# Kernel tuning notes

Measured on AMD Instinct MI355X. Metric: run time of the kernel, lower is better.

## Reference

```python
import math
import jax, jax.numpy as jnp
import numpy as np

B, CIN, COUT, K, S = 2, 64, 64, 3, 18  # batch, channels, kernel size per dim, spatial size per dim


def setup_inputs() -> dict:
    key = jax.random.key(0)
    k1, k2 = jax.random.split(key)
    inputs = jax.random.normal(k1, (B, CIN, S, S, S, S), dtype=jnp.float32)
    std = 1.0 / math.sqrt(CIN * K ** 4)  # matches init_weight: 1/sqrt(in_channels * n_offsets)
    kernel = jax.random.uniform(k2, (K ** 4, CIN, COUT), dtype=jnp.float32, minval=-std, maxval=std)
    return {"inputs": inputs, "kernel": kernel}


def reference(inputs, kernel):
    # kernel: [k0*k1*k2*k3, Cin, Cout], offsets enumerated row-major over the 4 kernel dims.
    # Equivalent to the per-offset matmul + shift-accumulate in conv4d (valid padding,
    # stride=1, dilation=1), expressed as a single 4-spatial-dim XLA convolution.
    cin, cout = kernel.shape[1], kernel.shape[2]
    w = kernel.reshape(K, K, K, K, cin, cout).transpose(5, 4, 0, 1, 2, 3)  # OIWXYZ
    out = jax.lax.conv_general_dilated(
        inputs, w,
        window_strides=(1, 1, 1, 1),
        padding='VALID',
        rhs_dilation=(1, 1, 1, 1),
        dimension_numbers=('NCWXYZ', 'OIWXYZ', 'NCWXYZ'),
    )  # [B, Cout, 16, 16, 16, 16]
    return out
```

## Files before the change

### kernel.cpp

```cpp
#include <hip/hip_runtime.h>


typedef __attribute__((ext_vector_type(8))) short bf16x8;
typedef __attribute__((ext_vector_type(4))) float f32x4;
typedef __attribute__((ext_vector_type(8))) unsigned short ushort8;
typedef unsigned short u16;
typedef unsigned int u32;

#define S_OFF_BYTES 663552u
#define WS_NEEDED   27537408u

__device__ __forceinline__ u16 f2bf(float f) {
    u32 u = __float_as_uint(f);
    u += 0x7FFFu + ((u >> 16) & 1u);
    return (u16)(u >> 16);
}

__global__ __launch_bounds__(256) void wprep(const float* __restrict__ ker, u16* __restrict__ wg) {
    const int g = blockIdx.x * 256 + threadIdx.x;
    const int l = g & 63, ks = (g >> 6) & 1, rt = (g >> 7) & 3, off = g >> 9;
    const int co  = rt * 16 + (l & 15);
    const int ci0 = ks * 32 + (l >> 4) * 8;
    const float* p = ker + (size_t)off * 4096 + co;
    ushort8 v;
#pragma unroll
    for (int e = 0; e < 8; ++e) v[e] = f2bf(p[(size_t)(ci0 + e) * 64]);
    *(ushort8*)(wg + (size_t)g * 8) = v;
}

__global__ __launch_bounds__(256) void sprep(const float* __restrict__ in, u16* __restrict__ s) {
    __shared__ u16 L[64 * 330];
    const int blk = blockIdx.x;
    const int b = blk / 324, wx = blk - b * 324;
    const float* src = in + (size_t)b * 6718464 + (wx / 18) * 5832 + (wx % 18) * 324;
    const int t = threadIdx.x;
    for (int i = t; i < 5184; i += 256) {
        const int ci = i / 81, j = i - ci * 81;
        float4 v = *(const float4*)(src + (size_t)ci * 104976 + j * 4);
        u32* q = (u32*)&L[ci * 330 + j * 4];
        q[0] = f2bf(v.x) | ((u32)f2bf(v.y) << 16);
        q[1] = f2bf(v.z) | ((u32)f2bf(v.w) << 16);
    }
    __syncthreads();
    u16* dst = s + (size_t)blk * 20736;
    for (int i = t; i < 2592; i += 256) {
        const int ks = i / 1296, r4 = i - ks * 1296;
        const int rem = r4 >> 2, g = r4 & 3;
        ushort8 v;
#pragma unroll
        for (int e = 0; e < 8; ++e) v[e] = L[(ks * 32 + g * 8 + e) * 330 + rem];
        const int gp = g ^ ((rem >> 1) & 3);
        *(ushort8*)(dst + ks * 10368 + rem * 32 + gp * 8) = v;
    }
}

__global__ __launch_bounds__(256, 2)
void conv4d_main(const u16* __restrict__ wg, const u16* __restrict__ s, float* __restrict__ out) {
    __shared__ u16 T[2][324 * 32];

    const int bid = blockIdx.x;
    const int bs  = (bid & 7) * 64 + (bid >> 3);
    const int b   = bs >> 8;
    const int w   = (bs >> 4) & 15;
    const int x   = bs & 15;

    const int t  = threadIdx.x, wv = t >> 6, l = t & 63;
    const int lg = l >> 4, ll = l & 15;

    f32x4 acc[4][4];
#pragma unroll
    for (int i = 0; i < 4; ++i)
#pragma unroll
        for (int j = 0; j < 4; ++j) acc[i][j] = (f32x4){0.f, 0.f, 0.f, 0.f};

    const u16* sb = s + (size_t)(b * 324 + w * 18 + x) * 20736;

#define STAGE(p, bufi)                                                               \
    do {                                                                             \
        const int kwx_ = (p) >> 1, ks_ = (p) & 1;                                    \
        const int kw_ = kwx_ / 3, kx_ = kwx_ - kw_ * 3;                              \
        const u16* src_ = sb + (size_t)(kw_ * 18 + kx_) * 20736 + ks_ * 10368;       \
        for (int i_ = t; i_ < 1296; i_ += 256)                                       \
            __builtin_amdgcn_global_load_lds(                                        \
                (const __attribute__((address_space(1))) u32*)(src_ + i_ * 8),       \
                (__attribute__((address_space(3))) u32*)&T[bufi][i_ * 8], 16, 0, 0); \
    } while (0)

    STAGE(0, 0);
    __syncthreads();

    int buf = 0;
    for (int p = 0; p < 18; ++p) {
        if (p + 1 < 18) STAGE(p + 1, buf ^ 1);

        const int kwx = p >> 1, ks = p & 1;
        const u16* wo = wg + (size_t)(kwx * 9) * 4096 + ks * 512;
        const u16* Tb = T[buf];

        bf16x8 a[4][4];
#pragma unroll
        for (int i = 0; i < 3; ++i)
#pragma unroll
            for (int rt = 0; rt < 4; ++rt)
                a[i][rt] = *(const bf16x8*)(wo + (size_t)i * 4096 + (size_t)rt * 1024 + l * 8);

#pragma unroll
        for (int sub = 0; sub < 9; ++sub) {
            if (sub + 3 < 9) {
                const u16* wn = wo + (size_t)(sub + 3) * 4096;
#pragma unroll
                for (int rt = 0; rt < 4; ++rt)
                    a[(sub + 3) & 3][rt] = *(const bf16x8*)(wn + (size_t)rt * 1024 + l * 8);
            }
            const int ky = sub / 3, kz = sub - ky * 3;
            bf16x8 bfr[4];
#pragma unroll
            for (int ct = 0; ct < 4; ++ct) {
                const int rem = (4 * wv + ct + ky) * 18 + ll + kz;
                bfr[ct] = *(const bf16x8*)&Tb[rem * 32 + ((lg ^ ((rem >> 1) & 3)) << 3)];
            }
            __builtin_amdgcn_s_setprio(1);
#pragma unroll
            for (int ct = 0; ct < 4; ++ct)
#pragma unroll
                for (int rt = 0; rt < 4; ++rt)
                    acc[rt][ct] = __builtin_amdgcn_mfma_f32_16x16x32_bf16(
                        a[sub & 3][rt], bfr[ct], acc[rt][ct], 0, 0, 0);
            __builtin_amdgcn_s_setprio(0);
        }
        __syncthreads();
        buf ^= 1;
    }
#undef STAGE

    float* ob = out + (size_t)b * 4194304 + (size_t)w * 4096 + (size_t)x * 256;
#pragma unroll
    for (int rt = 0; rt < 4; ++rt) {
        const int co0 = rt * 16 + 4 * lg;
#pragma unroll
        for (int ct = 0; ct < 4; ++ct) {
            const int base = (4 * wv + ct) * 16 + ll;
#pragma unroll
            for (int r = 0; r < 4; ++r)
                ob[(size_t)(co0 + r) * 65536 + base] = acc[rt][ct][r];
        }
    }
}

__global__ __launch_bounds__(512, 2)
void conv4d_mfma(const float* __restrict__ in, const float* __restrict__ ker,
                 float* __restrict__ out) {
    __shared__ unsigned short T[18 * 18 * 64];
    __shared__ unsigned short Wt[2][64 * 64];
    const int bx = blockIdx.x;
    const int b = bx >> 8, wsp = (bx >> 4) & 15, x = bx & 15;
    const int t = threadIdx.x, wv = t >> 6, l = t & 63;
    const int lg = l >> 4, ll = l & 15;
    const float* inb = in + (size_t)b * 6718464 + wsp * 5832 + x * 324;
    f32x4 acc[4][2];
#pragma unroll
    for (int i = 0; i < 4; ++i)
#pragma unroll
        for (int j = 0; j < 2; ++j) acc[i][j] = (f32x4){0.f, 0.f, 0.f, 0.f};
#pragma unroll
    for (int f0 = 0; f0 < 4096; f0 += 512) {
        const int f = f0 + t, ci = f >> 6, co = f & 63;
        Wt[0][co * 64 + ((((ci >> 3) ^ (co & 7)) << 3) | (ci & 7))] = f2bf(ker[f]);
    }
    for (int off = 0; off < 81; ++off) {
        const int sub = off % 9;
        if (sub == 0) {
            const int kw = off / 27, kx = (off / 9) % 3;
            const float* p = inb + kw * 5832 + kx * 324;
            for (int f = t; f < 18 * 18 * 64; f += 512) {
                const int ci = f / 324, rem = f - ci * 324, zp = rem % 18;
                T[rem * 64 + ((((ci >> 3) ^ (zp & 7)) << 3) | (ci & 7))] =
                    f2bf(p[(size_t)ci * 104976 + rem]);
            }
        }
        if (off + 1 < 81) {
            const float* p = ker + (off + 1) * 4096;
            unsigned short* wb = Wt[(off + 1) & 1];
#pragma unroll
            for (int f0 = 0; f0 < 4096; f0 += 512) {
                const int f = f0 + t, ci = f >> 6, co = f & 63;
                wb[co * 64 + ((((ci >> 3) ^ (co & 7)) << 3) | (ci & 7))] = f2bf(p[f]);
            }
        }
        if (sub == 0) __syncthreads();
        const int ky = sub / 3, kz = sub - ky * 3;
        const int zp = ll + kz, zs = zp & 7;
#pragma unroll
        for (int ks = 0; ks < 2; ++ks) {
            bf16x8 af[4];
#pragma unroll
            for (int rt = 0; rt < 4; ++rt)
                af[rt] = *(const bf16x8*)&Wt[off & 1][(rt * 16 + ll) * 64 + (((lg + 4 * ks) ^ (ll & 7)) << 3)];
#pragma unroll
            for (int ct = 0; ct < 2; ++ct) {
                const int rem = (2 * wv + ct + ky) * 18 + zp;
                const bf16x8 bfr = *(const bf16x8*)&T[rem * 64 + (((lg + 4 * ks) ^ zs) << 3)];
#pragma unroll
                for (int rt = 0; rt < 4; ++rt)
                    acc[rt][ct] = __builtin_amdgcn_mfma_f32_16x16x32_bf16(af[rt], bfr, acc[rt][ct], 0, 0, 0);
            }
        }
        __syncthreads();
    }
    float* ob = out + (size_t)b * 4194304 + wsp * 4096 + x * 256;
#pragma unroll
    for (int rt = 0; rt < 4; ++rt) {
        const int co0 = rt * 16 + 4 * lg;
#pragma unroll
        for (int ct = 0; ct < 2; ++ct) {
            const int base = (2 * wv + ct) * 16 + ll;
#pragma unroll
            for (int r = 0; r < 4; ++r)
                ob[(size_t)(co0 + r) * 65536 + base] = acc[rt][ct][r];
        }
    }
}

extern "C" void kernel_launch(void* const* d_in, const int* in_sizes, int n_in,
                              void* d_out, int out_size, void* d_ws, size_t ws_size,
                              hipStream_t stream) {
    const float* in  = (const float*)d_in[0];
    const float* ker = (const float*)d_in[1];
    float* out = (float*)d_out;
    if (ws_size >= (size_t)WS_NEEDED) {
        u16* wg = (u16*)d_ws;
        u16* s  = (u16*)((char*)d_ws + S_OFF_BYTES);
        wprep<<<dim3(162), dim3(256), 0, stream>>>(ker, wg);
        sprep<<<dim3(648), dim3(256), 0, stream>>>(in, s);
        conv4d_main<<<dim3(512), dim3(256), 0, stream>>>(wg, s, out);
    } else {
        conv4d_mfma<<<dim3(512), dim3(512), 0, stream>>>(in, ker, out);
    }
}
```

Baseline: 99.26 us.

## Split channel halves across two wave groups with staggered 4-slot staging and LDS reduction

Doubles the conv4d_main block to 512 threads, with waves 0-3 handling the first input-channel half and waves 4-7 the second. The two groups are staggered by one stage over a 4-slot LDS ring, and each barrier step stages two slices. At the end the second group writes its partial accumulators to LDS and the first group adds them before storing. This aims to double the waves available to hide load and MFMA latency per block, at the cost of more LDS per block, an extra reduction pass, and idle waves in the first and last steps.

```diff
diff --git a/kernel.cpp b/kernel.cpp
--- a/kernel.cpp
+++ b/kernel.cpp
@@ -54,9 +54,9 @@
     }
 }
 
-__global__ __launch_bounds__(256, 2)
+__global__ __launch_bounds__(512, 4)
 void conv4d_main(const u16* __restrict__ wg, const u16* __restrict__ s, float* __restrict__ out) {
-    __shared__ u16 T[2][324 * 32];
+    __shared__ u16 R[4][324 * 32];
 
     const int bid = blockIdx.x;
     const int bs  = (bid & 7) * 64 + (bid >> 3);
@@ -64,8 +64,10 @@
     const int w   = (bs >> 4) & 15;
     const int x   = bs & 15;
 
-    const int t  = threadIdx.x, wv = t >> 6, l = t & 63;
-    const int lg = l >> 4, ll = l & 15;
+    const int tid = threadIdx.x, wv = tid >> 6, l = tid & 63;
+    const int ks  = wv >> 2;
+    const int g   = wv & 3;
+    const int lg  = l >> 4, ll = l & 15;
 
     f32x4 acc[4][4];
 #pragma unroll
@@ -75,74 +77,91 @@
 
     const u16* sb = s + (size_t)(b * 324 + w * 18 + x) * 20736;
 
-#define STAGE(p, bufi)                                                               \
+#define STAGE_H(h)                                                                   \
     do {                                                                             \
-        const int kwx_ = (p) >> 1, ks_ = (p) & 1;                                    \
-        const int kw_ = kwx_ / 3, kx_ = kwx_ - kw_ * 3;                              \
-        const u16* src_ = sb + (size_t)(kw_ * 18 + kx_) * 20736 + ks_ * 10368;       \
-        for (int i_ = t; i_ < 1296; i_ += 256)                                       \
-            __builtin_amdgcn_global_load_lds(                                        \
-                (const __attribute__((address_space(1))) u32*)(src_ + i_ * 8),       \
-                (__attribute__((address_space(3))) u32*)&T[bufi][i_ * 8], 16, 0, 0); \
+        if ((h) <= 17) {                                                             \
+            const int kwx_ = (h) >> 1, ksh_ = (h) & 1;                               \
+            const int kw_ = kwx_ / 3, kx_ = kwx_ - kw_ * 3;                          \
+            const u16* src_ = sb + (size_t)(kw_ * 18 + kx_) * 20736 + ksh_ * 10368;  \
+            u16* dst_ = &R[(h) & 3][0];                                              \
+            for (int i_ = tid; i_ < 1296; i_ += 512)                                 \
+                __builtin_amdgcn_global_load_lds(                                    \
+                    (const __attribute__((address_space(1))) u32*)(src_ + i_ * 8),   \
+                    (__attribute__((address_space(3))) u32*)(dst_ + i_ * 8),         \
+                    16, 0, 0);                                                       \
+        }                                                                            \
     } while (0)
 
-    STAGE(0, 0);
+    STAGE_H(0);
     __syncthreads();
 
-    int buf = 0;
-    for (int p = 0; p < 18; ++p) {
-        if (p + 1 < 18) STAGE(p + 1, buf ^ 1);
-
-        const int kwx = p >> 1, ks = p & 1;
-        const u16* wo = wg + (size_t)(kwx * 9) * 4096 + ks * 512;
-        const u16* Tb = T[buf];
-
-        bf16x8 a[4][4];
-#pragma unroll
-        for (int i = 0; i < 3; ++i)
+    for (int t = 0; t < 10; ++t) {
+        STAGE_H(2 * t + 1);
+        STAGE_H(2 * t + 2);
+
+        const int h = 2 * t - ks;
+        if (h >= 0 && h <= 17) {
+            const int kwx = h >> 1;
+            const u16* Tb = R[h & 3];
+            const u16* wo = wg + (size_t)(kwx * 9) * 4096 + ks * 512;
+
+            bf16x8 a[2][4];
 #pragma unroll
             for (int rt = 0; rt < 4; ++rt)
-                a[i][rt] = *(const bf16x8*)(wo + (size_t)i * 4096 + (size_t)rt * 1024 + l * 8);
-
-#pragma unroll
-        for (int sub = 0; sub < 9; ++sub) {
-            if (sub + 3 < 9) {
-                const u16* wn = wo + (size_t)(sub + 3) * 4096;
-#pragma unroll
-                for (int rt = 0; rt < 4; ++rt)
-                    a[(sub + 3) & 3][rt] = *(const bf16x8*)(wn + (size_t)rt * 1024 + l * 8);
-            }
-            const int ky = sub / 3, kz = sub - ky * 3;
-            bf16x8 bfr[4];
+                a[0][rt] = *(const bf16x8*)(wo + (size_t)rt * 1024 + l * 8);
+
+#pragma unroll
+            for (int sub = 0; sub < 9; ++sub) {
+                if (sub + 1 < 9) {
+                    const u16* wn = wo + (size_t)(sub + 1) * 4096;
+#pragma unroll
+                    for (int rt = 0; rt < 4; ++rt)
+                        a[(sub + 1) & 1][rt] = *(const bf16x8*)(wn + (size_t)rt * 1024 + l * 8);
+                }
+                const int ky = sub / 3, kz = sub - ky * 3;
+                bf16x8 bfr[4];
+#pragma unroll
+                for (int ct = 0; ct < 4; ++ct) {
+                    const int rem = (4 * g + ct + ky) * 18 + ll + kz;
+                    bfr[ct] = *(const bf16x8*)&Tb[rem * 32 + ((lg ^ ((rem >> 1) & 3)) << 3)];
+                }
+                __builtin_amdgcn_s_setprio(1);
+#pragma unroll
+                for (int ct = 0; ct < 4; ++ct)
+#pragma unroll
+                    for (int rt = 0; rt < 4; ++rt)
+                        acc[rt][ct] = __builtin_amdgcn_mfma_f32_16x16x32_bf16(
+                            a[sub & 1][rt], bfr[ct], acc[rt][ct], 0, 0, 0);
+                __builtin_amdgcn_s_setprio(0);
+            }
+        }
+        __syncthreads();
+    }
+#undef STAGE_H
+
+    float* rbuf = (float*)&R[0][0];
+    if (ks == 1) {
+#pragma unroll
+        for (int rt = 0; rt < 4; ++rt)
+#pragma unroll
+            for (int ct = 0; ct < 4; ++ct)
+                *(f32x4*)&rbuf[g * 4096 + (rt * 4 + ct) * 256 + l * 4] = acc[rt][ct];
+    }
+    __syncthreads();
+    if (ks == 0) {
+        float* ob = out + (size_t)b * 4194304 + (size_t)w * 4096 + (size_t)x * 256;
+#pragma unroll
+        for (int rt = 0; rt < 4; ++rt) {
+            const int co0 = rt * 16 + 4 * lg;
 #pragma unroll
             for (int ct = 0; ct < 4; ++ct) {
-                const int rem = (4 * wv + ct + ky) * 18 + ll + kz;
-                bfr[ct] = *(const bf16x8*)&Tb[rem * 32 + ((lg ^ ((rem >> 1) & 3)) << 3)];
-            }
-            __builtin_amdgcn_s_setprio(1);
-#pragma unroll
-            for (int ct = 0; ct < 4; ++ct)
-#pragma unroll
-                for (int rt = 0; rt < 4; ++rt)
-                    acc[rt][ct] = __builtin_amdgcn_mfma_f32_16x16x32_bf16(
-                        a[sub & 3][rt], bfr[ct], acc[rt][ct], 0, 0, 0);
-            __builtin_amdgcn_s_setprio(0);
-        }
-        __syncthreads();
-        buf ^= 1;
-    }
-#undef STAGE
-
-    float* ob = out + (size_t)b * 4194304 + (size_t)w * 4096 + (size_t)x * 256;
-#pragma unroll
-    for (int rt = 0; rt < 4; ++rt) {
-        const int co0 = rt * 16 + 4 * lg;
-#pragma unroll
-        for (int ct = 0; ct < 4; ++ct) {
-            const int base = (4 * wv + ct) * 16 + ll;
-#pragma unroll
-            for (int r = 0; r < 4; ++r)
-                ob[(size_t)(co0 + r) * 65536 + base] = acc[rt][ct][r];
+                f32x4 v = *(const f32x4*)&rbuf[g * 4096 + (rt * 4 + ct) * 256 + l * 4];
+                v = v + acc[rt][ct];
+                const int base = (4 * g + ct) * 16 + ll;
+#pragma unroll
+                for (int r = 0; r < 4; ++r)
+                    ob[(size_t)(co0 + r) * 65536 + base] = v[r];
+            }
         }
     }
 }
@@ -232,7 +251,7 @@
         u16* s  = (u16*)((char*)d_ws + S_OFF_BYTES);
         wprep<<<dim3(162), dim3(256), 0, stream>>>(ker, wg);
         sprep<<<dim3(648), dim3(256), 0, stream>>>(in, s);
-        conv4d_main<<<dim3(512), dim3(256), 0, stream>>>(wg, s, out);
+        conv4d_main<<<dim3(512), dim3(512), 0, stream>>>(wg, s, out);
     } else {
         conv4d_mfma<<<dim3(512), dim3(512), 0, stream>>>(in, ker, out);
     }
```

Measured after the change: 99.04 us. Within noise of the previous version (-0.2%).

## Triple-buffer LDS input staging with explicit vmcnt waits instead of syncthreads

Applied to the files above, without the earlier changes.

Replaces the double-buffered shared-memory tile with a three-slot ring. Each phase now prefetches the slab two phases ahead instead of one. The full `__syncthreads` is replaced by a partial `s_waitcnt vmcnt` plus a raw `s_barrier`, so the block waits only for the slab about to be consumed. Each wave now issues a fixed, unrolled set of direct-to-LDS loads over its own quarter of the tile. This deepens latency hiding for the global-to-LDS copies, at the cost of about 20 KB more LDS per block and a hand-tuned vmcnt count that depends on the exact number of in-flight loads.

```diff
diff --git a/kernel.cpp b/kernel.cpp
--- a/kernel.cpp
+++ b/kernel.cpp
@@ -56,7 +56,7 @@
 
 __global__ __launch_bounds__(256, 2)
 void conv4d_main(const u16* __restrict__ wg, const u16* __restrict__ s, float* __restrict__ out) {
-    __shared__ u16 T[2][324 * 32];
+    __shared__ u16 R[3][324 * 32];
 
     const int bid = blockIdx.x;
     const int bs  = (bid & 7) * 64 + (bid >> 3);
@@ -75,27 +75,39 @@
 
     const u16* sb = s + (size_t)(b * 324 + w * 18 + x) * 20736;
 
-#define STAGE(p, bufi)                                                               \
-    do {                                                                             \
-        const int kwx_ = (p) >> 1, ks_ = (p) & 1;                                    \
-        const int kw_ = kwx_ / 3, kx_ = kwx_ - kw_ * 3;                              \
-        const u16* src_ = sb + (size_t)(kw_ * 18 + kx_) * 20736 + ks_ * 10368;       \
-        for (int i_ = t; i_ < 1296; i_ += 256)                                       \
-            __builtin_amdgcn_global_load_lds(                                        \
-                (const __attribute__((address_space(1))) u32*)(src_ + i_ * 8),       \
-                (__attribute__((address_space(3))) u32*)&T[bufi][i_ * 8], 16, 0, 0); \
+#define STAGE_U(h, slot)                                                                 \
+    do {                                                                                 \
+        const int kwx_ = (h) >> 1, ks_ = (h) & 1;                                        \
+        const int kw_ = kwx_ / 3, kx_ = kwx_ - kw_ * 3;                                  \
+        const u16* src_ = sb + (size_t)(kw_ * 18 + kx_) * 20736 + ks_ * 10368;           \
+        const int base_ = wv * 324;                                                      \
+        _Pragma("unroll")                                                                \
+        for (int k_ = 0; k_ < 5; ++k_) {                                                 \
+            const int i_ = base_ + k_ * 64 + l;                                          \
+            __builtin_amdgcn_global_load_lds(                                            \
+                (const __attribute__((address_space(1))) u32*)(src_ + (size_t)i_ * 8),   \
+                (__attribute__((address_space(3))) u32*)&R[slot][i_ * 8], 16, 0, 0);     \
+        }                                                                                \
+        if (l < 4) {                                                                     \
+            const int i_ = base_ + 320 + l;                                              \
+            __builtin_amdgcn_global_load_lds(                                            \
+                (const __attribute__((address_space(1))) u32*)(src_ + (size_t)i_ * 8),   \
+                (__attribute__((address_space(3))) u32*)&R[slot][i_ * 8], 16, 0, 0);     \
+        }                                                                                \
     } while (0)
 
-    STAGE(0, 0);
-    __syncthreads();
-
-    int buf = 0;
+    STAGE_U(0, 0);
+    STAGE_U(1, 1);
+    asm volatile("s_waitcnt vmcnt(6)" ::: "memory");
+    __builtin_amdgcn_sched_barrier(0);
+    __builtin_amdgcn_s_barrier();
+
     for (int p = 0; p < 18; ++p) {
-        if (p + 1 < 18) STAGE(p + 1, buf ^ 1);
+        if (p + 2 < 18) STAGE_U(p + 2, (p + 2) % 3);
 
         const int kwx = p >> 1, ks = p & 1;
         const u16* wo = wg + (size_t)(kwx * 9) * 4096 + ks * 512;
-        const u16* Tb = T[buf];
+        const u16* Tb = R[p % 3];
 
         bf16x8 a[4][4];
 #pragma unroll
@@ -128,10 +140,15 @@
                         a[sub & 3][rt], bfr[ct], acc[rt][ct], 0, 0, 0);
             __builtin_amdgcn_s_setprio(0);
         }
-        __syncthreads();
-        buf ^= 1;
-    }
-#undef STAGE
+
+        if (p < 17) {
+            if (p < 16) asm volatile("s_waitcnt vmcnt(6)" ::: "memory");
+            else        asm volatile("s_waitcnt vmcnt(0)" ::: "memory");
+            __builtin_amdgcn_sched_barrier(0);
+            __builtin_amdgcn_s_barrier();
+        }
+    }
+#undef STAGE_U
 
     float* ob = out + (size_t)b * 4194304 + (size_t)w * 4096 + (size_t)x * 256;
 #pragma unroll
```

Result: no change. 100.9 us (+1.7%).
